# Optimization experiments

Measured on AMD Instinct MI355X. Metric: run time of the kernel, lower is better.

The kernel has to match this reference:

```python
import jax, jax.numpy as jnp
import numpy as np

N_NODES = 100000
N_EDGES = 1600000
IN_CH = 64
HID = 64
N_CLASSES = 10
N_GRAPHS = 64


def setup_inputs() -> dict:
    key = jax.random.key(0)
    ks = jax.random.split(key, 12)
    x = jax.random.normal(ks[0], (N_NODES, IN_CH), dtype=jnp.float32)
    edge_index = jax.random.randint(ks[1], (2, N_EDGES), 0, N_NODES, dtype=jnp.int64)
    batch = jnp.sort(jax.random.randint(ks[2], (N_NODES,), 0, N_GRAPHS, dtype=jnp.int64))
    def glorot(k, shape):
        lim = 1.0 / np.sqrt(shape[1])
        return jax.random.uniform(k, shape, dtype=jnp.float32, minval=-lim, maxval=lim)
    # GraphConv layer 1: lin_rel (with bias) and lin_root (no bias)
    W1_rel = glorot(ks[3], (HID, IN_CH))
    W1_root = glorot(ks[4], (HID, IN_CH))
    b1 = glorot(ks[5], (1, IN_CH))[0, :HID] * 0 + glorot(ks[5], (HID, 1))[:, 0]
    # GraphConv layer 2
    W2_rel = glorot(ks[6], (HID, HID))
    W2_root = glorot(ks[7], (HID, HID))
    b2 = glorot(ks[8], (HID, 1))[:, 0]
    # final classifier Linear
    W_lin = glorot(ks[9], (N_CLASSES, HID))
    b_lin = glorot(ks[10], (N_CLASSES, 1))[:, 0]
    return {
        "x": x, "edge_index": edge_index, "batch": batch,
        "W1_rel": W1_rel, "W1_root": W1_root, "b1": b1,
        "W2_rel": W2_rel, "W2_root": W2_root, "b2": b2,
        "W_lin": W_lin, "b_lin": b_lin,
    }


def _graph_conv(x, src, dst, W_rel, W_root, b):
    # PyG GraphConv: out_i = W_rel @ (sum_{j->i} x_j) + b + W_root @ x_i
    agg = jax.ops.segment_sum(x[src], dst, num_segments=N_NODES)  # [N, C]
    return agg @ W_rel.T + x @ W_root.T + b


def reference(x, edge_index, batch, W1_rel, W1_root, b1, W2_rel, W2_root, b2, W_lin, b_lin):
    src, dst = edge_index[0], edge_index[1]
    h = jax.nn.relu(_graph_conv(x, src, dst, W1_rel, W1_root, b1))
    h = jax.nn.relu(_graph_conv(h, src, dst, W2_rel, W2_root, b2))
    # global mean pool over graph ids
    sums = jax.ops.segment_sum(h, batch, num_segments=N_GRAPHS)          # [G, H]
    counts = jax.ops.segment_sum(jnp.ones((h.shape[0],), h.dtype), batch, num_segments=N_GRAPHS)
    pooled = sums / jnp.maximum(counts, 1.0)[:, None]
    return pooled @ W_lin.T + b_lin  # [G, num_classes]
```

## Files before the change

kernel.cpp:

```cpp
#include <hip/hip_runtime.h>

typedef unsigned short u16;
typedef __attribute__((ext_vector_type(8))) short bf16x8;
typedef __attribute__((ext_vector_type(4))) float f32x4;

constexpr int CH = 64;
constexpr int NG = 64;
constexpr int NC = 10;
constexpr int SHIFT = 9;
constexpr int BW = 1 << SHIFT;
constexpr int EPW = 4096;
constexpr int PT = EPW / 256;

__device__ __forceinline__ void f4add(float4& a, const float4 v) {
    a.x += v.x; a.y += v.y; a.z += v.z; a.w += v.w;
}
__device__ __forceinline__ u16 f2bf(float f) {
    unsigned u = __float_as_uint(f);
    u = (u + 0x7FFFu + ((u >> 16) & 1u)) >> 16;
    return (u16)u;
}
__device__ __forceinline__ void bfacc(float4& a, unsigned lo, unsigned hi) {
    a.x += __uint_as_float(lo << 16);
    a.y += __uint_as_float(lo & 0xFFFF0000u);
    a.z += __uint_as_float(hi << 16);
    a.w += __uint_as_float(hi & 0xFFFF0000u);
}

__device__ __forceinline__ void bucket_body(int bid,
                                            const int* __restrict__ src,
                                            const int* __restrict__ dst,
                                            int* __restrict__ bcnt,
                                            int* __restrict__ bbuf,
                                            int nb, int cap, int n_edges)
{
    __shared__ int hist[256];
    __shared__ int cur[256];
    int t = threadIdx.x;
    int e0 = bid * EPW;
    int e1 = min(e0 + EPW, n_edges);
    if (t < nb) hist[t] = 0;
    __syncthreads();
    int base = e0 + t * PT;
    bool full = (base + PT <= e1);
    int db[PT];
    if (full) {
        const int4* p = (const int4*)(dst + base);
#pragma unroll
        for (int j = 0; j < PT / 4; ++j) {
            int4 v = p[j];
            db[4 * j + 0] = v.x; db[4 * j + 1] = v.y;
            db[4 * j + 2] = v.z; db[4 * j + 3] = v.w;
        }
#pragma unroll
        for (int j = 0; j < PT; ++j) atomicAdd(&hist[db[j] >> SHIFT], 1);
    } else {
        for (int i = base; i < e1; ++i) atomicAdd(&hist[dst[i] >> SHIFT], 1);
    }
    __syncthreads();
    if (t < nb) cur[t] = atomicAdd(&bcnt[t], hist[t]);
    __syncthreads();
    if (full) {
        int sb[PT];
        const int4* p = (const int4*)(src + base);
#pragma unroll
        for (int j = 0; j < PT / 4; ++j) {
            int4 v = p[j];
            sb[4 * j + 0] = v.x; sb[4 * j + 1] = v.y;
            sb[4 * j + 2] = v.z; sb[4 * j + 3] = v.w;
        }
#pragma unroll
        for (int j = 0; j < PT; ++j) {
            int d = db[j];
            int b = d >> SHIFT;
            int pos = atomicAdd(&cur[b], 1);
            if (pos < cap)
                bbuf[(size_t)b * cap + pos] = sb[j] | ((d & (BW - 1)) << 17);
        }
    } else {
        for (int i = base; i < e1; ++i) {
            int d = dst[i];
            int b = d >> SHIFT;
            int pos = atomicAdd(&cur[b], 1);
            if (pos < cap)
                bbuf[(size_t)b * cap + pos] = src[i] | ((d & (BW - 1)) << 17);
        }
    }
}

template<bool BF16IN>
__device__ __forceinline__ void xform_body(int bid, const void* in_,
                                           const float* __restrict__ Wrel,
                                           const float* __restrict__ Wroot,
                                           const float* __restrict__ bias,
                                           u16* __restrict__ Y,
                                           u16* R, int n, int ngroups)
{
    if (bid == 0 && threadIdx.x < 64)
        Y[(size_t)n * CH + threadIdx.x] = 0;

    int lane = threadIdx.x & 63;
    int lr = lane & 15;
    int g  = lane >> 4;

    bf16x8 wf[2][4][2];
    const float* Wm[2] = { Wrel, Wroot };
#pragma unroll
    for (int m = 0; m < 2; ++m)
#pragma unroll
        for (int t = 0; t < 4; ++t)
#pragma unroll
            for (int kt = 0; kt < 2; ++kt) {
                const float* p = Wm[m] + (16 * t + lr) * CH + 32 * kt + 8 * g;
                bf16x8 v;
#pragma unroll
                for (int j = 0; j < 8; ++j) v[j] = (short)f2bf(p[j]);
                wf[m][t][kt] = v;
            }
    float bvt[4];
#pragma unroll
    for (int t = 0; t < 4; ++t) bvt[t] = bias[16 * t + lr];

    int wid = bid * 4 + (threadIdx.x >> 6);
#pragma unroll
    for (int gi = 0; gi < 2; ++gi) {
        int grp = wid * 2 + gi;
        if (grp >= ngroups) return;
        int gbase = grp * 16;
        int arow = gbase + lr;
        if (arow >= n) arow = n - 1;

        bf16x8 af[2];
#pragma unroll
        for (int kt = 0; kt < 2; ++kt) {
            if (BF16IN) {
                const u16* hp = (const u16*)in_ + (size_t)arow * CH + kt * 32 + 8 * g;
                af[kt] = *(const bf16x8*)hp;
            } else {
                const float* xp = (const float*)in_ + (size_t)arow * CH + kt * 32 + 8 * g;
                bf16x8 v;
#pragma unroll
                for (int j = 0; j < 8; ++j) v[j] = (short)f2bf(xp[j]);
                af[kt] = v;
            }
        }

        f32x4 z = { 0.f, 0.f, 0.f, 0.f };
        f32x4 aY[4] = { z, z, z, z };
        f32x4 aR[4] = { z, z, z, z };
#pragma unroll
        for (int kt = 0; kt < 2; ++kt)
#pragma unroll
            for (int t = 0; t < 4; ++t) {
                aY[t] = __builtin_amdgcn_mfma_f32_16x16x32_bf16(af[kt], wf[0][t][kt], aY[t], 0, 0, 0);
                aR[t] = __builtin_amdgcn_mfma_f32_16x16x32_bf16(af[kt], wf[1][t][kt], aR[t], 0, 0, 0);
            }

#pragma unroll
        for (int t = 0; t < 4; ++t)
#pragma unroll
            for (int r = 0; r < 4; ++r) {
                int node = gbase + 4 * g + r;
                if (node < n) {
                    Y[(size_t)node * CH + 16 * t + lr] = f2bf(aY[t][r]);
                    R[(size_t)node * CH + 16 * t + lr] = f2bf(aR[t][r] + bvt[t]);
                }
            }
    }
}

__global__ __launch_bounds__(256) void k_bx(const int* __restrict__ src,
                                            const int* __restrict__ dst,
                                            int* __restrict__ bcnt,
                                            int* __restrict__ bbuf,
                                            int nb, int cap, int n_edges,
                                            const float* __restrict__ x,
                                            const float* __restrict__ Wrel,
                                            const float* __restrict__ Wroot,
                                            const float* __restrict__ bias,
                                            u16* __restrict__ Y,
                                            u16* R, int n, int ngroups, int xoff)
{
    if ((int)blockIdx.x < xoff)
        bucket_body(blockIdx.x, src, dst, bcnt, bbuf, nb, cap, n_edges);
    else
        xform_body<false>(blockIdx.x - xoff, x, Wrel, Wroot, bias, Y, R, n, ngroups);
}

__global__ __launch_bounds__(256) void k_xform2(const u16* in_,
                                                const float* __restrict__ Wrel,
                                                const float* __restrict__ Wroot,
                                                const float* __restrict__ bias,
                                                u16* __restrict__ Y,
                                                u16* R, int n, int ngroups)
{
    xform_body<true>(blockIdx.x, in_, Wrel, Wroot, bias, Y, R, n, ngroups);
}

__global__ __launch_bounds__(256) void k_build(const int* __restrict__ bbuf,
                                               const int* __restrict__ bcnt,
                                               int* __restrict__ rowptr,
                                               int* __restrict__ csr,
                                               int nb, int cap, int n)
{
    __shared__ int sc[256];
    __shared__ int hist[BW];
    __shared__ int cur[BW];
    __shared__ int psum[256];
    int b = blockIdx.x;
    int t = threadIdx.x;
    int v = (t < nb) ? min(bcnt[t], cap) : 0;
    sc[t] = v;
    __syncthreads();
    for (int off = 1; off < 256; off <<= 1) {
        int u = (t >= off) ? sc[t - off] : 0;
        __syncthreads();
        sc[t] += u;
        __syncthreads();
    }
    if (b == 0 && t == nb - 1) rowptr[n] = sc[t];
    int cnt = min(bcnt[b], cap);
    int base = sc[b] - cnt;
    __syncthreads();
    const int* mybuf = bbuf + (size_t)b * cap;
    hist[t] = 0; hist[t + 256] = 0;
    __syncthreads();
    for (int i = t; i < cnt; i += 256)
        atomicAdd(&hist[mybuf[i] >> 17], 1);
    __syncthreads();
    int h0 = hist[2 * t], h1 = hist[2 * t + 1];
    int ps = h0 + h1;
    psum[t] = ps;
    __syncthreads();
    for (int off = 1; off < 256; off <<= 1) {
        int u = (t >= off) ? psum[t - off] : 0;
        __syncthreads();
        psum[t] += u;
        __syncthreads();
    }
    int e0 = psum[t] - ps;
    int nodeBase = b * BW;
    cur[2 * t]     = base + e0;
    cur[2 * t + 1] = base + e0 + h0;
    if (nodeBase + 2 * t < n)     rowptr[nodeBase + 2 * t]     = base + e0;
    if (nodeBase + 2 * t + 1 < n) rowptr[nodeBase + 2 * t + 1] = base + e0 + h0;
    __syncthreads();
    for (int i = t; i < cnt; i += 256) {
        int vv = mybuf[i];
        int pos = atomicAdd(&cur[vv >> 17], 1);
        csr[pos] = vv & 0x1FFFF;
    }
}

template<bool POOL>
__global__ __launch_bounds__(256) void k_gather5(const u16* __restrict__ Y,
                                                 const int* __restrict__ rowptr,
                                                 const int* __restrict__ csr,
                                                 u16* RO,
                                                 const int* __restrict__ batch,
                                                 float* __restrict__ sums,
                                                 int n, int chunk)
{
    int lane = threadIdx.x & 63;
    int grp = lane >> 4, sub = lane & 15;
    int wid = blockIdx.x * 4 + (threadIdx.x >> 6);
    int nb = wid * chunk, ne = min(nb + chunk, n);
    if (nb >= n) return;
    float4 run = make_float4(0, 0, 0, 0);
    int gcur = -1;
    int e0 = rowptr[nb];
    for (int node = nb; node < ne; ++node) {
        int e1 = rowptr[node + 1];
        uint2 pr = *(const uint2*)(RO + (size_t)node * CH + sub * 4);
        float4 a0 = make_float4(0, 0, 0, 0), a1 = a0;
        int e = e0;
        for (; e + 16 <= e1; e += 16) {
            int s0 = csr[e + grp],      s1 = csr[e + 4 + grp];
            int s2 = csr[e + 8 + grp],  s3 = csr[e + 12 + grp];
            uint2 p0 = *(const uint2*)(Y + (size_t)s0 * CH + sub * 4);
            uint2 p1 = *(const uint2*)(Y + (size_t)s1 * CH + sub * 4);
            uint2 p2 = *(const uint2*)(Y + (size_t)s2 * CH + sub * 4);
            uint2 p3 = *(const uint2*)(Y + (size_t)s3 * CH + sub * 4);
            bfacc(a0, p0.x, p0.y); bfacc(a1, p1.x, p1.y);
            bfacc(a0, p2.x, p2.y); bfacc(a1, p3.x, p3.y);
        }
        if (e < e1) {
            int s0 = (e + grp      < e1) ? csr[e + grp]      : n;
            int s1 = (e + 4 + grp  < e1) ? csr[e + 4 + grp]  : n;
            int s2 = (e + 8 + grp  < e1) ? csr[e + 8 + grp]  : n;
            int s3 = (e + 12 + grp < e1) ? csr[e + 12 + grp] : n;
            uint2 p0 = *(const uint2*)(Y + (size_t)s0 * CH + sub * 4);
            uint2 p1 = *(const uint2*)(Y + (size_t)s1 * CH + sub * 4);
            uint2 p2 = *(const uint2*)(Y + (size_t)s2 * CH + sub * 4);
            uint2 p3 = *(const uint2*)(Y + (size_t)s3 * CH + sub * 4);
            bfacc(a0, p0.x, p0.y); bfacc(a1, p1.x, p1.y);
            bfacc(a0, p2.x, p2.y); bfacc(a1, p3.x, p3.y);
        }
        e0 = e1;
        f4add(a0, a1);
        a0.x += __shfl_xor(a0.x, 16); a0.y += __shfl_xor(a0.y, 16);
        a0.z += __shfl_xor(a0.z, 16); a0.w += __shfl_xor(a0.w, 16);
        a0.x += __shfl_xor(a0.x, 32); a0.y += __shfl_xor(a0.y, 32);
        a0.z += __shfl_xor(a0.z, 32); a0.w += __shfl_xor(a0.w, 32);
        float4 r = make_float4(0, 0, 0, 0);
        bfacc(r, pr.x, pr.y);
        float4 h;
        h.x = fmaxf(a0.x + r.x, 0.f); h.y = fmaxf(a0.y + r.y, 0.f);
        h.z = fmaxf(a0.z + r.z, 0.f); h.w = fmaxf(a0.w + r.w, 0.f);
        if (!POOL) {
            if (grp == 0) {
                uint2 o;
                o.x = (unsigned)f2bf(h.x) | ((unsigned)f2bf(h.y) << 16);
                o.y = (unsigned)f2bf(h.z) | ((unsigned)f2bf(h.w) << 16);
                *(uint2*)(RO + (size_t)node * CH + sub * 4) = o;
            }
        } else {
            int g = batch[node];
            if (g != gcur) {
                if (gcur >= 0 && grp == 0) {
                    float* s = sums + gcur * CH + sub * 4;
                    atomicAdd(s + 0, run.x); atomicAdd(s + 1, run.y);
                    atomicAdd(s + 2, run.z); atomicAdd(s + 3, run.w);
                }
                run = make_float4(0, 0, 0, 0);
                gcur = g;
            }
            f4add(run, h);
        }
    }
    if (POOL && gcur >= 0 && grp == 0) {
        float* s = sums + gcur * CH + sub * 4;
        atomicAdd(s + 0, run.x); atomicAdd(s + 1, run.y);
        atomicAdd(s + 2, run.z); atomicAdd(s + 3, run.w);
    }
}

__global__ __launch_bounds__(64) void k_final2(const float* __restrict__ sums,
                                               const int* __restrict__ batch,
                                               const float* __restrict__ Wlin,
                                               const float* __restrict__ blin,
                                               float* __restrict__ out, int n_nodes)
{
    int g = blockIdx.x;
    int l = threadIdx.x;
    int lo = 0, hi = n_nodes;
    while (lo < hi) { int mid = (lo + hi) >> 1; if (batch[mid] < g) lo = mid + 1; else hi = mid; }
    int lb = lo;
    lo = 0; hi = n_nodes;
    while (lo < hi) { int mid = (lo + hi) >> 1; if (batch[mid] < g + 1) lo = mid + 1; else hi = mid; }
    int cnt = lo - lb;
    float inv = 1.0f / fmaxf((float)cnt, 1.0f);
    float v = sums[g * CH + l] * inv;
#pragma unroll
    for (int c = 0; c < NC; ++c) {
        float p = v * Wlin[c * CH + l];
        p += __shfl_xor(p, 1);  p += __shfl_xor(p, 2);  p += __shfl_xor(p, 4);
        p += __shfl_xor(p, 8);  p += __shfl_xor(p, 16); p += __shfl_xor(p, 32);
        if (l == 0) out[g * NC + c] = p + blin[c];
    }
}

extern "C" void kernel_launch(void* const* d_in, const int* in_sizes, int n_in,
                              void* d_out, int out_size, void* d_ws, size_t ws_size,
                              hipStream_t stream)
{
    const float* x      = (const float*)d_in[0];
    const int*   ei     = (const int*)d_in[1];
    const int*   batch  = (const int*)d_in[2];
    const float* W1rel  = (const float*)d_in[3];
    const float* W1root = (const float*)d_in[4];
    const float* b1     = (const float*)d_in[5];
    const float* W2rel  = (const float*)d_in[6];
    const float* W2root = (const float*)d_in[7];
    const float* b2     = (const float*)d_in[8];
    const float* Wlin   = (const float*)d_in[9];
    const float* blin   = (const float*)d_in[10];
    float* out = (float*)d_out;

    int n_nodes = in_sizes[0] / CH;
    int n_edges = in_sizes[1] / 2;
    const int* src = ei;
    const int* dst = ei + n_edges;

    int nb  = (n_nodes + BW - 1) >> SHIFT;
    int cap = n_edges / nb + 2048;

    u16*   Ybf    = (u16*)d_ws;
    u16*   Rbf    = Ybf + (size_t)(n_nodes + 1) * CH;
    int*   rowptr = (int*)(Rbf + (size_t)n_nodes * CH);
    int*   csr    = rowptr + (n_nodes + 1);
    int*   bbuf   = csr + n_edges + 32;
    int*   bcnt   = bbuf + (size_t)nb * cap;
    float* sums   = (float*)(bcnt + 256);

    int ngroups16 = (n_nodes + 15) / 16;
    int xblocks = (ngroups16 + 7) / 8;
    int b1blocks = (n_edges + EPW - 1) / EPW;

    int waves = 2048 * 4;
    int chunk = (n_nodes + waves - 1) / waves;

    hipMemsetAsync(bcnt, 0, 256 * sizeof(int), stream);
    k_bx<<<b1blocks + xblocks, 256, 0, stream>>>(src, dst, bcnt, bbuf, nb, cap, n_edges,
                                                 x, W1rel, W1root, b1,
                                                 Ybf, Rbf, n_nodes, ngroups16, b1blocks);
    k_build<<<nb, 256, 0, stream>>>(bbuf, bcnt, rowptr, csr, nb, cap, n_nodes);

    k_gather5<false><<<2048, 256, 0, stream>>>(Ybf, rowptr, csr, Rbf,
                                               batch, sums, n_nodes, chunk);

    k_xform2<<<xblocks, 256, 0, stream>>>(Rbf, W2rel, W2root, b2,
                                          Ybf, Rbf, n_nodes, ngroups16);
    hipMemsetAsync(sums, 0, NG * CH * sizeof(float), stream);
    k_gather5<true><<<2048, 256, 0, stream>>>(Ybf, rowptr, csr, Rbf,
                                              batch, sums, n_nodes, chunk);

    k_final2<<<NG, 64, 0, stream>>>(sums, batch, Wlin, blin, out, n_nodes);
}
```

Measured before the change: 206.5 us.

## Split layer-1 transform across bucket and CSR-build kernels, fold sums memset

The first-layer feature transform is split so that about three fifths of its blocks run alongside the edge bucketing kernel and the rest run alongside the CSR build kernel. The CSR build becomes a device function inside a combined kernel. The aim is to fill idle CUs during the small build launch, which has only one block per bucket. The separate memset of the pooling sums is folded into build block 0, removing one launch. This adds shared-memory use to the xform blocks in the combined kernel and makes the split ratio hard-coded.

```diff
diff --git a/kernel.cpp b/kernel.cpp
--- a/kernel.cpp
+++ b/kernel.cpp
@@ -94,9 +94,9 @@
                                            const float* __restrict__ Wroot,
                                            const float* __restrict__ bias,
                                            u16* __restrict__ Y,
-                                           u16* R, int n, int ngroups)
-{
-    if (bid == 0 && threadIdx.x < 64)
+                                           u16* R, int n, int g0, int gend)
+{
+    if (g0 == 0 && bid == 0 && threadIdx.x < 64)
         Y[(size_t)n * CH + threadIdx.x] = 0;
 
     int lane = threadIdx.x & 63;
@@ -124,8 +124,8 @@
     int wid = bid * 4 + (threadIdx.x >> 6);
 #pragma unroll
     for (int gi = 0; gi < 2; ++gi) {
-        int grp = wid * 2 + gi;
-        if (grp >= ngroups) return;
+        int grp = g0 + wid * 2 + gi;
+        if (grp >= gend) return;
         int gbase = grp * 16;
         int arow = gbase + lr;
         if (arow >= n) arow = n - 1;
@@ -169,22 +169,100 @@
     }
 }
 
-__global__ __launch_bounds__(256) void k_bx(const int* __restrict__ src,
-                                            const int* __restrict__ dst,
-                                            int* __restrict__ bcnt,
-                                            int* __restrict__ bbuf,
-                                            int nb, int cap, int n_edges,
-                                            const float* __restrict__ x,
-                                            const float* __restrict__ Wrel,
-                                            const float* __restrict__ Wroot,
-                                            const float* __restrict__ bias,
-                                            u16* __restrict__ Y,
-                                            u16* R, int n, int ngroups, int xoff)
+__device__ __forceinline__ void build_body(int b,
+                                           const int* __restrict__ bbuf,
+                                           const int* __restrict__ bcnt,
+                                           int* __restrict__ rowptr,
+                                           int* __restrict__ csr,
+                                           float* __restrict__ sums,
+                                           int nb, int cap, int n)
+{
+    __shared__ int sc[256];
+    __shared__ int hist[BW];
+    __shared__ int cur[BW];
+    __shared__ int psum[256];
+    int t = threadIdx.x;
+    if (b == 0) {
+        for (int i = t; i < NG * CH; i += 256) sums[i] = 0.f;
+    }
+    int v = (t < nb) ? min(bcnt[t], cap) : 0;
+    sc[t] = v;
+    __syncthreads();
+    for (int off = 1; off < 256; off <<= 1) {
+        int u = (t >= off) ? sc[t - off] : 0;
+        __syncthreads();
+        sc[t] += u;
+        __syncthreads();
+    }
+    if (b == 0 && t == nb - 1) rowptr[n] = sc[t];
+    int cnt = min(bcnt[b], cap);
+    int base = sc[b] - cnt;
+    __syncthreads();
+    const int* mybuf = bbuf + (size_t)b * cap;
+    hist[t] = 0; hist[t + 256] = 0;
+    __syncthreads();
+    for (int i = t; i < cnt; i += 256)
+        atomicAdd(&hist[mybuf[i] >> 17], 1);
+    __syncthreads();
+    int h0 = hist[2 * t], h1 = hist[2 * t + 1];
+    int ps = h0 + h1;
+    psum[t] = ps;
+    __syncthreads();
+    for (int off = 1; off < 256; off <<= 1) {
+        int u = (t >= off) ? psum[t - off] : 0;
+        __syncthreads();
+        psum[t] += u;
+        __syncthreads();
+    }
+    int e0 = psum[t] - ps;
+    int nodeBase = b * BW;
+    cur[2 * t]     = base + e0;
+    cur[2 * t + 1] = base + e0 + h0;
+    if (nodeBase + 2 * t < n)     rowptr[nodeBase + 2 * t]     = base + e0;
+    if (nodeBase + 2 * t + 1 < n) rowptr[nodeBase + 2 * t + 1] = base + e0 + h0;
+    __syncthreads();
+    for (int i = t; i < cnt; i += 256) {
+        int vv = mybuf[i];
+        int pos = atomicAdd(&cur[vv >> 17], 1);
+        csr[pos] = vv & 0x1FFFF;
+    }
+}
+
+__global__ __launch_bounds__(256) void k_b1x(const int* __restrict__ src,
+                                             const int* __restrict__ dst,
+                                             int* __restrict__ bcnt,
+                                             int* __restrict__ bbuf,
+                                             int nb, int cap, int n_edges,
+                                             const float* __restrict__ x,
+                                             const float* __restrict__ Wrel,
+                                             const float* __restrict__ Wroot,
+                                             const float* __restrict__ bias,
+                                             u16* __restrict__ Y,
+                                             u16* R, int n, int gA, int xoff)
 {
     if ((int)blockIdx.x < xoff)
         bucket_body(blockIdx.x, src, dst, bcnt, bbuf, nb, cap, n_edges);
     else
-        xform_body<false>(blockIdx.x - xoff, x, Wrel, Wroot, bias, Y, R, n, ngroups);
+        xform_body<false>(blockIdx.x - xoff, x, Wrel, Wroot, bias, Y, R, n, 0, gA);
+}
+
+__global__ __launch_bounds__(256) void k_b2x(const int* __restrict__ bbuf,
+                                             const int* __restrict__ bcnt,
+                                             int* __restrict__ rowptr,
+                                             int* __restrict__ csr,
+                                             float* __restrict__ sums,
+                                             int nb, int cap,
+                                             const float* __restrict__ x,
+                                             const float* __restrict__ Wrel,
+                                             const float* __restrict__ Wroot,
+                                             const float* __restrict__ bias,
+                                             u16* __restrict__ Y,
+                                             u16* R, int n, int gA, int gend)
+{
+    if ((int)blockIdx.x < nb)
+        build_body(blockIdx.x, bbuf, bcnt, rowptr, csr, sums, nb, cap, n);
+    else
+        xform_body<false>(blockIdx.x - nb, x, Wrel, Wroot, bias, Y, R, n, gA, gend);
 }
 
 __global__ __launch_bounds__(256) void k_xform2(const u16* in_,
@@ -194,62 +272,7 @@
                                                 u16* __restrict__ Y,
                                                 u16* R, int n, int ngroups)
 {
-    xform_body<true>(blockIdx.x, in_, Wrel, Wroot, bias, Y, R, n, ngroups);
-}
-
-__global__ __launch_bounds__(256) void k_build(const int* __restrict__ bbuf,
-                                               const int* __restrict__ bcnt,
-                                               int* __restrict__ rowptr,
-                                               int* __restrict__ csr,
-                                               int nb, int cap, int n)
-{
-    __shared__ int sc[256];
-    __shared__ int hist[BW];
-    __shared__ int cur[BW];
-    __shared__ int psum[256];
-    int b = blockIdx.x;
-    int t = threadIdx.x;
-    int v = (t < nb) ? min(bcnt[t], cap) : 0;
-    sc[t] = v;
-    __syncthreads();
-    for (int off = 1; off < 256; off <<= 1) {
-        int u = (t >= off) ? sc[t - off] : 0;
-        __syncthreads();
-        sc[t] += u;
-        __syncthreads();
-    }
-    if (b == 0 && t == nb - 1) rowptr[n] = sc[t];
-    int cnt = min(bcnt[b], cap);
-    int base = sc[b] - cnt;
-    __syncthreads();
-    const int* mybuf = bbuf + (size_t)b * cap;
-    hist[t] = 0; hist[t + 256] = 0;
-    __syncthreads();
-    for (int i = t; i < cnt; i += 256)
-        atomicAdd(&hist[mybuf[i] >> 17], 1);
-    __syncthreads();
-    int h0 = hist[2 * t], h1 = hist[2 * t + 1];
-    int ps = h0 + h1;
-    psum[t] = ps;
-    __syncthreads();
-    for (int off = 1; off < 256; off <<= 1) {
-        int u = (t >= off) ? psum[t - off] : 0;
-        __syncthreads();
-        psum[t] += u;
-        __syncthreads();
-    }
-    int e0 = psum[t] - ps;
-    int nodeBase = b * BW;
-    cur[2 * t]     = base + e0;
-    cur[2 * t + 1] = base + e0 + h0;
-    if (nodeBase + 2 * t < n)     rowptr[nodeBase + 2 * t]     = base + e0;
-    if (nodeBase + 2 * t + 1 < n) rowptr[nodeBase + 2 * t + 1] = base + e0 + h0;
-    __syncthreads();
-    for (int i = t; i < cnt; i += 256) {
-        int vv = mybuf[i];
-        int pos = atomicAdd(&cur[vv >> 17], 1);
-        csr[pos] = vv & 0x1FFFF;
-    }
+    xform_body<true>(blockIdx.x, in_, Wrel, Wroot, bias, Y, R, n, 0, ngroups);
 }
 
 template<bool POOL>
@@ -397,21 +420,28 @@
     int xblocks = (ngroups16 + 7) / 8;
     int b1blocks = (n_edges + EPW - 1) / EPW;
 
+    int xfA = xblocks * 3 / 5;
+    if (xfA < 1) xfA = 1;
+    int gA = xfA * 8;
+    if (gA > ngroups16) { gA = ngroups16; xfA = (gA + 7) / 8; }
+    int xfB = (ngroups16 - gA + 7) / 8;
+
     int waves = 2048 * 4;
     int chunk = (n_nodes + waves - 1) / waves;
 
     hipMemsetAsync(bcnt, 0, 256 * sizeof(int), stream);
-    k_bx<<<b1blocks + xblocks, 256, 0, stream>>>(src, dst, bcnt, bbuf, nb, cap, n_edges,
-                                                 x, W1rel, W1root, b1,
-                                                 Ybf, Rbf, n_nodes, ngroups16, b1blocks);
-    k_build<<<nb, 256, 0, stream>>>(bbuf, bcnt, rowptr, csr, nb, cap, n_nodes);
+    k_b1x<<<b1blocks + xfA, 256, 0, stream>>>(src, dst, bcnt, bbuf, nb, cap, n_edges,
+                                              x, W1rel, W1root, b1,
+                                              Ybf, Rbf, n_nodes, gA, b1blocks);
+    k_b2x<<<nb + xfB, 256, 0, stream>>>(bbuf, bcnt, rowptr, csr, sums, nb, cap,
+                                        x, W1rel, W1root, b1,
+                                        Ybf, Rbf, n_nodes, gA, ngroups16);
 
     k_gather5<false><<<2048, 256, 0, stream>>>(Ybf, rowptr, csr, Rbf,
                                                batch, sums, n_nodes, chunk);
 
     k_xform2<<<xblocks, 256, 0, stream>>>(Rbf, W2rel, W2root, b2,
                                           Ybf, Rbf, n_nodes, ngroups16);
-    hipMemsetAsync(sums, 0, NG * CH * sizeof(float), stream);
     k_gather5<true><<<2048, 256, 0, stream>>>(Ybf, rowptr, csr, Rbf,
                                               batch, sums, n_nodes, chunk);
 
```

After: 198.9 us, median of 2. 3.7% less time.
